# Kernel tuning notes

Hardware: AMD Instinct MI355X
Metric: run time of the kernel (lower is better)

The kernel has to match this reference:

```python
import jax, jax.numpy as jnp
import numpy as np

GAMMA = 1.0
ALPHA = 1.0
B, C = 32768, 1000


def setup_inputs() -> dict:
    key = jax.random.key(0)
    k1, k2 = jax.random.split(key)
    logits = jax.random.normal(k1, (B, C), dtype=jnp.float32)
    target = jax.random.randint(k2, (B,), 0, C, dtype=jnp.int64)
    return {"logits": logits, "target": target}


def reference(logits, target):
    # softmax probabilities (log_softmax().exp() in the original)
    p = jax.nn.softmax(logits, axis=-1)                      # [B, C]
    y = jax.nn.one_hot(target, logits.shape[-1], dtype=p.dtype)  # [B, C]
    # self-adjusting decay: (1 - p)^alpha * p
    pa = (1.0 - p) ** ALPHA * p                              # [B, C]
    numerator = pa * y                                       # [B, C]
    denominator = pa + y                                     # [B, C]  (squared=False)
    # per-class dice loss, summed over classes, averaged by C (vectorized
    # version of the original per-class Python loop; mask is all-ones since
    # ignore_index=None)
    per_class = 1.0 - (2.0 * numerator + GAMMA) / (denominator + GAMMA)  # [B, C]
    loss = per_class.sum(axis=-1) / logits.shape[-1]         # [B]
    return loss.mean()                                       # reduction='mean'
```

## Files before the change

### kernel.cpp

```cpp
#include <hip/hip_runtime.h>
#include <math.h>

#define NROWS 32768
#define NCLS  1000
#define NV4   250
#define WAVES_PER_BLK 16
#define NBLK  (NROWS / WAVES_PER_BLK)
#define LOG2E 1.4426950408889634f

typedef float f32x4 __attribute__((ext_vector_type(4)));

__global__ __launch_bounds__(1024) void dice_onepass_kernel(
    const float* __restrict__ logits,
    const int*   __restrict__ target,
    unsigned*    __restrict__ slotA,
    unsigned*    __restrict__ slotB,
    float*       __restrict__ out)
{
    const int wave = threadIdx.x >> 6;
    const int lane = threadIdx.x & 63;
    const int row  = blockIdx.x * WAVES_PER_BLK + wave;

    const f32x4* src = (const f32x4*)(logits + (size_t)row * NCLS);
    const int   t  = target[row];
    const float xt = logits[(size_t)row * NCLS + t];

    float e[16];
    float ssum = 0.0f;
    #pragma unroll
    for (int s = 0; s < 4; ++s) {
        const int idx = lane + (s << 6);
        f32x4 v4;
        if (idx < NV4) {
            v4 = src[idx];
        } else {
            v4 = (f32x4){-INFINITY, -INFINITY, -INFINITY, -INFINITY};
        }
        const float e0 = __builtin_amdgcn_exp2f(v4.x * LOG2E);
        const float e1 = __builtin_amdgcn_exp2f(v4.y * LOG2E);
        const float e2 = __builtin_amdgcn_exp2f(v4.z * LOG2E);
        const float e3 = __builtin_amdgcn_exp2f(v4.w * LOG2E);
        e[4*s+0] = e0; e[4*s+1] = e1; e[4*s+2] = e2; e[4*s+3] = e3;
        ssum += (e0 + e1) + (e2 + e3);
    }
    #pragma unroll
    for (int off = 32; off; off >>= 1) ssum += __shfl_xor(ssum, off);
    const float inv = __builtin_amdgcn_rcpf(ssum);

    float acc = 0.0f;
    #pragma unroll
    for (int i = 0; i < 16; ++i) {
        const float p  = e[i] * inv;
        const float pa = __builtin_fmaf(-p, p, p);
        acc += pa * __builtin_amdgcn_rcpf(pa + 1.0f);
    }
    #pragma unroll
    for (int off = 32; off; off >>= 1) acc += __shfl_xor(acc, off);

    const float et  = __builtin_amdgcn_exp2f(xt * LOG2E);
    const float pt  = et * inv;
    const float pat = __builtin_fmaf(-pt, pt, pt);
    const float corr = (1.0f - pat) * __builtin_amdgcn_rcpf(pat + 2.0f)
                     - pat * __builtin_amdgcn_rcpf(pat + 1.0f);

    __shared__ float sm[WAVES_PER_BLK];
    if (lane == 0) sm[wave] = (acc + corr) * (1.0f / NCLS);
    __syncthreads();

    if (threadIdx.x < 64) {
        float v = (lane < WAVES_PER_BLK) ? sm[lane] : 0.0f;
        #pragma unroll
        for (int off = 8; off; off >>= 1) v += __shfl_xor(v, off);
        if (lane == 0) {
            const unsigned bits = __float_as_uint(v);
            atomicExch(&slotA[blockIdx.x], bits);
            atomicExch(&slotB[blockIdx.x], ~bits);
        }
    }

    if (blockIdx.x != 0) return;

    const int tid = threadIdx.x;
    float v0, v1;
    {
        unsigned a, b;
        do {
            a = __hip_atomic_load(&slotA[tid], __ATOMIC_RELAXED,
                                  __HIP_MEMORY_SCOPE_AGENT);
            b = __hip_atomic_load(&slotB[tid], __ATOMIC_RELAXED,
                                  __HIP_MEMORY_SCOPE_AGENT);
            if (b == ~a) break;
            __builtin_amdgcn_s_sleep(2);
        } while (true);
        v0 = __uint_as_float(a);
        do {
            a = __hip_atomic_load(&slotA[tid + 1024], __ATOMIC_RELAXED,
                                  __HIP_MEMORY_SCOPE_AGENT);
            b = __hip_atomic_load(&slotB[tid + 1024], __ATOMIC_RELAXED,
                                  __HIP_MEMORY_SCOPE_AGENT);
            if (b == ~a) break;
            __builtin_amdgcn_s_sleep(2);
        } while (true);
        v1 = __uint_as_float(a);
    }

    __shared__ float red[1024];
    red[tid] = v0 + v1;
    __syncthreads();
    #pragma unroll
    for (int off = 512; off; off >>= 1) {
        if (tid < off) red[tid] += red[tid + off];
        __syncthreads();
    }
    if (tid == 0) out[0] = red[0] * (1.0f / NROWS);
}

extern "C" void kernel_launch(void* const* d_in, const int* in_sizes, int n_in,
                              void* d_out, int out_size, void* d_ws, size_t ws_size,
                              hipStream_t stream)
{
    const float* logits = (const float*)d_in[0];
    const int*   target = (const int*)d_in[1];
    float*    out   = (float*)d_out;
    unsigned* slotA = (unsigned*)d_ws;
    unsigned* slotB = slotA + NBLK;

    dice_onepass_kernel<<<NBLK, 1024, 0, stream>>>(logits, target,
                                                   slotA, slotB, out);
}
```

Baseline: 25.79 us.

## Process four rows per wave and replace reciprocal with polynomial series

Each wave now handles four consecutive rows in a loop. This cuts the grid to a quarter of the blocks and shrinks the cross-block reduction that block 0 spin-waits on to 512 slots. The per-element pa/(1+pa) term now uses a truncated alternating series built from FMAs instead of a hardware reciprocal, and the wave shuffle reduction runs once for all four rows. The series is only accurate for small pa, which adds approximation error, and the sequential row loop may expose less memory-level parallelism on a bandwidth-bound kernel.

New measurement: 26.36 us. +2.2%, slower.

```diff
diff --git a/kernel.cpp b/kernel.cpp
--- a/kernel.cpp
+++ b/kernel.cpp
@@ -5,7 +5,8 @@
 #define NCLS  1000
 #define NV4   250
 #define WAVES_PER_BLK 16
-#define NBLK  (NROWS / WAVES_PER_BLK)
+#define ROWS_PER_WAVE 4
+#define NBLK  (NROWS / (WAVES_PER_BLK * ROWS_PER_WAVE))
 #define LOG2E 1.4426950408889634f
 
 typedef float f32x4 __attribute__((ext_vector_type(4)));
@@ -19,52 +20,62 @@
 {
     const int wave = threadIdx.x >> 6;
     const int lane = threadIdx.x & 63;
-    const int row  = blockIdx.x * WAVES_PER_BLK + wave;
+    const int rowBase = (blockIdx.x * WAVES_PER_BLK + wave) * ROWS_PER_WAVE;
 
-    const f32x4* src = (const f32x4*)(logits + (size_t)row * NCLS);
-    const int   t  = target[row];
-    const float xt = logits[(size_t)row * NCLS + t];
+    float wsum = 0.0f;
+    float csum = 0.0f;
 
-    float e[16];
-    float ssum = 0.0f;
+    for (int r = 0; r < ROWS_PER_WAVE; ++r) {
+        const int row = rowBase + r;
+        const f32x4* src = (const f32x4*)(logits + (size_t)row * NCLS);
+        const int   t  = target[row];
+        const float xt = logits[(size_t)row * NCLS + t];
+
+        float e[16];
+        float ssum = 0.0f;
+        #pragma unroll
+        for (int s = 0; s < 4; ++s) {
+            const int idx = lane + (s << 6);
+            f32x4 v4;
+            if (idx < NV4) {
+                v4 = src[idx];
+            } else {
+                v4 = (f32x4){-INFINITY, -INFINITY, -INFINITY, -INFINITY};
+            }
+            const float e0 = __builtin_amdgcn_exp2f(v4.x * LOG2E);
+            const float e1 = __builtin_amdgcn_exp2f(v4.y * LOG2E);
+            const float e2 = __builtin_amdgcn_exp2f(v4.z * LOG2E);
+            const float e3 = __builtin_amdgcn_exp2f(v4.w * LOG2E);
+            e[4*s+0] = e0; e[4*s+1] = e1; e[4*s+2] = e2; e[4*s+3] = e3;
+            ssum += (e0 + e1) + (e2 + e3);
+        }
+        #pragma unroll
+        for (int off = 32; off; off >>= 1) ssum += __shfl_xor(ssum, off);
+        const float inv = __builtin_amdgcn_rcpf(ssum);
+
+        #pragma unroll
+        for (int i = 0; i < 16; ++i) {
+            const float p  = e[i] * inv;
+            const float pa = __builtin_fmaf(-p, p, p);
+            const float s1 = 1.0f - pa;
+            const float s2 = __builtin_fmaf(-pa, s1, 1.0f);
+            const float s3 = __builtin_fmaf(-pa, s2, 1.0f);
+            wsum = __builtin_fmaf(pa, s3, wsum);
+        }
+
+        const float et  = __builtin_amdgcn_exp2f(xt * LOG2E);
+        const float pt  = et * inv;
+        const float pat = __builtin_fmaf(-pt, pt, pt);
+        csum += (1.0f - pat) * __builtin_amdgcn_rcpf(pat + 2.0f)
+              - pat * __builtin_amdgcn_rcpf(pat + 1.0f);
+    }
+
     #pragma unroll
-    for (int s = 0; s < 4; ++s) {
-        const int idx = lane + (s << 6);
-        f32x4 v4;
-        if (idx < NV4) {
-            v4 = src[idx];
-        } else {
-            v4 = (f32x4){-INFINITY, -INFINITY, -INFINITY, -INFINITY};
-        }
-        const float e0 = __builtin_amdgcn_exp2f(v4.x * LOG2E);
-        const float e1 = __builtin_amdgcn_exp2f(v4.y * LOG2E);
-        const float e2 = __builtin_amdgcn_exp2f(v4.z * LOG2E);
-        const float e3 = __builtin_amdgcn_exp2f(v4.w * LOG2E);
-        e[4*s+0] = e0; e[4*s+1] = e1; e[4*s+2] = e2; e[4*s+3] = e3;
-        ssum += (e0 + e1) + (e2 + e3);
-    }
-    #pragma unroll
-    for (int off = 32; off; off >>= 1) ssum += __shfl_xor(ssum, off);
-    const float inv = __builtin_amdgcn_rcpf(ssum);
-
-    float acc = 0.0f;
-    #pragma unroll
-    for (int i = 0; i < 16; ++i) {
-        const float p  = e[i] * inv;
-        const float pa = __builtin_fmaf(-p, p, p);
-        acc += pa * __builtin_amdgcn_rcpf(pa + 1.0f);
-    }
-    #pragma unroll
-    for (int off = 32; off; off >>= 1) acc += __shfl_xor(acc, off);
-
-    const float et  = __builtin_amdgcn_exp2f(xt * LOG2E);
-    const float pt  = et * inv;
-    const float pat = __builtin_fmaf(-pt, pt, pt);
-    const float corr = (1.0f - pat) * __builtin_amdgcn_rcpf(pat + 2.0f)
-                     - pat * __builtin_amdgcn_rcpf(pat + 1.0f);
+    for (int off = 32; off; off >>= 1) wsum += __shfl_xor(wsum, off);
+    const float waveTotal = (wsum + csum) * (1.0f / NCLS);
 
     __shared__ float sm[WAVES_PER_BLK];
-    if (lane == 0) sm[wave] = (acc + corr) * (1.0f / NCLS);
+    if (lane == 0) sm[wave] = waveTotal;
     __syncthreads();
 
     if (threadIdx.x < 64) {
@@ -81,8 +92,8 @@
     if (blockIdx.x != 0) return;
 
     const int tid = threadIdx.x;
-    float v0, v1;
-    {
+    float v0 = 0.0f;
+    if (tid < NBLK) {
         unsigned a, b;
         do {
             a = __hip_atomic_load(&slotA[tid], __ATOMIC_RELAXED,
@@ -93,22 +104,13 @@
             __builtin_amdgcn_s_sleep(2);
         } while (true);
         v0 = __uint_as_float(a);
-        do {
-            a = __hip_atomic_load(&slotA[tid + 1024], __ATOMIC_RELAXED,
-                                  __HIP_MEMORY_SCOPE_AGENT);
-            b = __hip_atomic_load(&slotB[tid + 1024], __ATOMIC_RELAXED,
-                                  __HIP_MEMORY_SCOPE_AGENT);
-            if (b == ~a) break;
-            __builtin_amdgcn_s_sleep(2);
-        } while (true);
-        v1 = __uint_as_float(a);
     }
 
-    __shared__ float red[1024];
-    red[tid] = v0 + v1;
+    __shared__ float red[NBLK];
+    if (tid < NBLK) red[tid] = v0;
     __syncthreads();
     #pragma unroll
-    for (int off = 512; off; off >>= 1) {
+    for (int off = NBLK / 2; off; off >>= 1) {
         if (tid < off) red[tid] += red[tid + off];
         __syncthreads();
     }
```
